# Performance work log

Measured on AMD Instinct MI355X. Metric: run time of the kernel, lower is better.

Reference implementation:

```python
import jax, jax.numpy as jnp
import numpy as np

NU = 3
NUM_MEM_TOKENS = 128
EPS = 1e-5


def dpfp(x, nu=NU):
    # x: [..., d] -> [..., 2*nu*d]; all outputs are >= 0
    x = jnp.concatenate([jax.nn.relu(x), jax.nn.relu(-x)], axis=-1)
    x_rolled = jnp.concatenate([jnp.roll(x, shift=j, axis=-1) for j in range(1, nu + 1)], axis=-1)
    x_repeat = jnp.concatenate([x] * nu, axis=-1)
    return x_repeat * x_rolled


def setup_inputs() -> dict:
    key = jax.random.key(0)
    ks = jax.random.split(key, 8)
    B, S, D, DM = 1, 16384, 2048, 64
    DK = 2 * NU * DM  # 384
    scale = 0.02
    return {
        "hidden_states": jax.random.normal(ks[0], (B, S, D), jnp.float32),
        "Wmq": jax.random.normal(ks[1], (DM, D), jnp.float32) * scale,
        "Wmk": jax.random.normal(ks[2], (DM, D), jnp.float32) * scale,
        "Wmv": jax.random.normal(ks[3], (D, D), jnp.float32) * scale,
        "Wmb_w": jax.random.normal(ks[4], (1, D), jnp.float32) * scale,
        "Wmb_b": jax.random.normal(ks[5], (1,), jnp.float32),
        "W_mem": jax.random.normal(ks[6], (B, DK, D), jnp.float32) * scale,
        "z": jax.random.uniform(ks[7], (B, DK), jnp.float32) + 0.1,
    }


def reference(hidden_states, Wmq, Wmk, Wmv, Wmb_w, Wmb_b, W_mem, z):
    # ---- associate (read from fast-weight memory) ----
    mq = dpfp(hidden_states @ Wmq.T)                       # [b,s,dk]
    num = jnp.einsum('ijk,ikt->ijt', mq, W_mem)            # [b,s,d]
    denom = jnp.einsum('ik,ijk->ij', z, mq)[..., None] + EPS
    hidden_states = num / denom + hidden_states

    # wrapped transformer layer modeled as identity
    out = hidden_states

    # ---- update_mem (write: recurrent outer-product accumulation) ----
    mem_tokens = out[:, -NUM_MEM_TOKENS:]                  # [b,m,d]
    mk = dpfp(mem_tokens @ Wmk.T)                          # [b,m,dk]
    new_mv = mem_tokens @ Wmv.T                            # [b,m,d]

    num2 = jnp.einsum('ijk,ikt->ijt', mk, W_mem)           # [b,m,d]
    denom2 = jnp.einsum('ij,ikj->ik', z, mk)[..., None] + EPS
    prev_mv = num2 / denom2

    mk_sq = jnp.sum(mk * mk, axis=-1)                      # ||mk||^2, [b,m]
    new_info_coef = 1.0 - denom2 / (mk_sq + EPS)[..., None]
    new_info_coef = jax.lax.stop_gradient(jnp.clip(new_info_coef, 0.0, 1.0))

    mv = new_mv - prev_mv
    mb = jax.nn.sigmoid(mem_tokens @ Wmb_w.T + Wmb_b)[..., 0]  # [b,m]
    associations = jnp.einsum('ijk,ijt,ij->ikt', mk, mv, mb)   # [b,dk,d]

    W_mem_new = W_mem + associations
    z_new = z + jnp.sum(new_info_coef * mk, axis=1)
    return out, W_mem_new, z_new
```

## Files before the change

kernel.cpp:

```cpp
#include <hip/hip_runtime.h>
#include <hip/hip_bf16.h>
#include <math.h>

#define S_ 16384
#define D_ 2048
#define DM_ 64
#define DK_ 384
#define NMEM_ 128
#define EPS_ 1e-5f

typedef __attribute__((ext_vector_type(8))) short bf16x8;
typedef __attribute__((ext_vector_type(8))) short s16x8;
typedef __attribute__((ext_vector_type(4))) float f32x4;
typedef unsigned short u16;

static __device__ __forceinline__ u16 f2bf(float x) {
    __hip_bfloat16 h = __float2bfloat16(x);
    return *reinterpret_cast<u16*>(&h);
}

static __device__ __forceinline__ void gload16(const void* g, void* l) {
    __builtin_amdgcn_global_load_lds(
        (const __attribute__((address_space(1))) unsigned int*)g,
        (__attribute__((address_space(3))) unsigned int*)l, 16, 0, 0);
}

__global__ __launch_bounds__(256) void k_qprep(const float* __restrict__ hs,
                                               const float* __restrict__ Wmq,
                                               const float* __restrict__ Wmv,
                                               const float* __restrict__ Wmem,
                                               const float* __restrict__ z,
                                               u16* __restrict__ Wmv_b,
                                               u16* __restrict__ WmT,
                                               u16* __restrict__ mq_b,
                                               float* __restrict__ denomv) {
    __shared__ float ts[32][33];
    __shared__ u16 As[32 * 128];
    __shared__ u16 Bs[64 * 128];
    __shared__ float xs[32][128];
    __shared__ float zs[DK_];
    const int bid = blockIdx.x;
    const int tid = threadIdx.x;
    if (bid < 4096) {
        size_t idx = ((size_t)bid * 256 + tid) * 4;
        float4 v = *reinterpret_cast<const float4*>(&Wmv[idx]);
        ushort4 p;
        p.x = f2bf(v.x); p.y = f2bf(v.y); p.z = f2bf(v.z); p.w = f2bf(v.w);
        *reinterpret_cast<ushort4*>(&Wmv_b[idx]) = p;
        return;
    }
    if (bid < 4864) {
        int t = bid - 4096;
        int c0 = (t & 63) * 32, k0 = (t >> 6) * 32;
        const int tx = tid & 31, ty = tid >> 5;
#pragma unroll
        for (int i = 0; i < 4; ++i)
            ts[ty + 8 * i][tx] = Wmem[(size_t)(k0 + ty + 8 * i) * D_ + c0 + tx];
        __syncthreads();
#pragma unroll
        for (int i = 0; i < 4; ++i)
            WmT[(size_t)(c0 + ty + 8 * i) * DK_ + k0 + tx] = f2bf(ts[tx][ty + 8 * i]);
        return;
    }
    const int r0 = (bid - 4864) * 32;
    const int lane = tid & 63, w = tid >> 6;
    const int lrow = lane & 15, lkg = lane >> 4;
    const int wr = w >> 1, wc = w & 1;
    for (int i = tid; i < DK_; i += 256) zs[i] = z[i];
    f32x4 acc[2];
    const f32x4 zero4 = {0.f, 0.f, 0.f, 0.f};
    acc[0] = zero4; acc[1] = zero4;
    for (int kc = 0; kc < D_ / 128; ++kc) {
#pragma unroll
        for (int i = 0; i < 4; ++i) {
            int flat4 = tid + 256 * i;
            int row = flat4 >> 5, c4 = flat4 & 31;
            const float4 v = *reinterpret_cast<const float4*>(
                &hs[(size_t)(r0 + row) * D_ + kc * 128 + c4 * 4]);
            int off = row * 128 + (((c4 >> 1) ^ (row & 7)) * 8) + (c4 & 1) * 4;
            ushort4 p;
            p.x = f2bf(v.x); p.y = f2bf(v.y); p.z = f2bf(v.z); p.w = f2bf(v.w);
            *reinterpret_cast<ushort4*>(&As[off]) = p;
        }
#pragma unroll
        for (int i = 0; i < 8; ++i) {
            int flat4 = tid + 256 * i;
            int row = flat4 >> 5, c4 = flat4 & 31;
            const float4 v = *reinterpret_cast<const float4*>(
                &Wmq[(size_t)row * D_ + kc * 128 + c4 * 4]);
            int off = row * 128 + (((c4 >> 1) ^ (row & 7)) * 8) + (c4 & 1) * 4;
            ushort4 p;
            p.x = f2bf(v.x); p.y = f2bf(v.y); p.z = f2bf(v.z); p.w = f2bf(v.w);
            *reinterpret_cast<ushort4*>(&Bs[off]) = p;
        }
        __syncthreads();
#pragma unroll
        for (int s = 0; s < 4; ++s) {
            int rl = wr * 16 + lrow;
            bf16x8 a_ = *reinterpret_cast<const bf16x8*>(
                &As[rl * 128 + (((s * 4 + lkg) ^ (rl & 7)) * 8)]);
#pragma unroll
            for (int n = 0; n < 2; ++n) {
                int cl = wc * 32 + n * 16 + lrow;
                bf16x8 b_ = *reinterpret_cast<const bf16x8*>(
                    &Bs[cl * 128 + (((s * 4 + lkg) ^ (cl & 7)) * 8)]);
                acc[n] = __builtin_amdgcn_mfma_f32_16x16x32_bf16(a_, b_, acc[n], 0, 0, 0);
            }
        }
        __syncthreads();
    }
#pragma unroll
    for (int n = 0; n < 2; ++n) {
        int col = wc * 32 + n * 16 + lrow;
#pragma unroll
        for (int r = 0; r < 4; ++r) {
            int row = wr * 16 + lkg * 4 + r;
            float q = acc[n][r];
            xs[row][col] = fmaxf(q, 0.f);
            xs[row][col + 64] = fmaxf(-q, 0.f);
        }
    }
    __syncthreads();
    {
        int row = tid >> 3, sub = tid & 7;
        float pd = 0.f;
#pragma unroll
        for (int c = 0; c < 6; ++c) {
            int base = sub * 48 + c * 8;
            int g = base >> 7;
            s16x8 pk;
#pragma unroll
            for (int e = 0; e < 8; ++e) {
                int m = base + e;
                int i = m & 127;
                float v = xs[row][i] * xs[row][(i - g - 1) & 127];
                pd += zs[m] * v;
                pk[e] = (short)f2bf(v);
            }
            *reinterpret_cast<s16x8*>(&mq_b[(size_t)(r0 + row) * DK_ + base]) = pk;
        }
        pd += __shfl_down(pd, 4, 8);
        pd += __shfl_down(pd, 2, 8);
        pd += __shfl_down(pd, 1, 8);
        if (sub == 0) denomv[r0 + row] = pd + EPS_;
    }
}

__global__ __launch_bounds__(256) void k_main(const float* __restrict__ hs,
                                              const u16* __restrict__ mq_b,
                                              const u16* __restrict__ WmT,
                                              const float* __restrict__ denomv,
                                              float* __restrict__ out) {
    __shared__ u16 At[128 * 64];
    __shared__ u16 Bt[128 * 64];
    __shared__ float dinv[128];
    const int bid = blockIdx.x;
    const int swz = (bid & 7) * 256 + (bid >> 3);
    const int r0 = (swz >> 4) * 128, c0 = (swz & 15) * 128;
    const int tid = threadIdx.x;
    const int lane = tid & 63, w = tid >> 6;
    const int lrow = lane & 15, lkg = lane >> 4;
    const int wr = w >> 1, wc = w & 1;
    if (tid < 128) dinv[tid] = 1.f / denomv[r0 + tid];
    f32x4 acc[4][4];
    const f32x4 zero4 = {0.f, 0.f, 0.f, 0.f};
#pragma unroll
    for (int m = 0; m < 4; ++m)
#pragma unroll
        for (int n = 0; n < 4; ++n) acc[m][n] = zero4;
    for (int kc = 0; kc < 6; ++kc) {
#pragma unroll
        for (int i = 0; i < 4; ++i) {
            int rr = w * 32 + i * 8 + (lane >> 3);
            int gg = (lane & 7) ^ (rr & 7);
            gload16(mq_b + (size_t)(r0 + rr) * DK_ + kc * 64 + gg * 8,
                    &At[(w * 32 + i * 8) * 64]);
            gload16(WmT + (size_t)(c0 + rr) * DK_ + kc * 64 + gg * 8,
                    &Bt[(w * 32 + i * 8) * 64]);
        }
        __syncthreads();
#pragma unroll
        for (int s = 0; s < 2; ++s) {
            bf16x8 af[4], bb[4];
#pragma unroll
            for (int m = 0; m < 4; ++m) {
                int rl = wr * 64 + m * 16 + lrow;
                af[m] = *reinterpret_cast<const bf16x8*>(
                    &At[rl * 64 + (((s * 4 + lkg) ^ (rl & 7)) * 8)]);
            }
#pragma unroll
            for (int n = 0; n < 4; ++n) {
                int cl = wc * 64 + n * 16 + lrow;
                bb[n] = *reinterpret_cast<const bf16x8*>(
                    &Bt[cl * 64 + (((s * 4 + lkg) ^ (cl & 7)) * 8)]);
            }
#pragma unroll
            for (int m = 0; m < 4; ++m)
#pragma unroll
                for (int n = 0; n < 4; ++n)
                    acc[m][n] = __builtin_amdgcn_mfma_f32_16x16x32_bf16(
                        af[m], bb[n], acc[m][n], 0, 0, 0);
        }
        __syncthreads();
    }
#pragma unroll
    for (int m = 0; m < 4; ++m)
#pragma unroll
        for (int n = 0; n < 4; ++n) {
            int colg = c0 + wc * 64 + n * 16 + lrow;
#pragma unroll
            for (int r = 0; r < 4; ++r) {
                int rowl = wr * 64 + m * 16 + lkg * 4 + r;
                size_t off = (size_t)(r0 + rowl) * D_ + colg;
                out[off] = acc[m][n][r] * dinv[rowl] + hs[off];
            }
        }
}

__global__ __launch_bounds__(256) void k_mk(const float* __restrict__ out,
                                            const float* __restrict__ Wmk,
                                            const float* __restrict__ Wmb_w,
                                            const float* __restrict__ Wmb_b,
                                            const float* __restrict__ z,
                                            float* __restrict__ mk_g,
                                            u16* __restrict__ mk_b,
                                            u16* __restrict__ mem_b,
                                            float* __restrict__ scal) {
    __shared__ float memRow[D_];
    __shared__ float qpart[4][64];
    __shared__ float xv[128];
    __shared__ float mks[DK_];
    __shared__ float red[256];
    const int j = blockIdx.x;
    const int tid = threadIdx.x;
    const float* mem = out + (size_t)(S_ - NMEM_ + j) * D_;
    const float4* mem4 = reinterpret_cast<const float4*>(mem);
    float4* mr4 = reinterpret_cast<float4*>(memRow);
#pragma unroll
    for (int i4 = tid; i4 < 512; i4 += 256) {
        float4 v = mem4[i4];
        mr4[i4] = v;
        ushort4 p;
        p.x = f2bf(v.x); p.y = f2bf(v.y); p.z = f2bf(v.z); p.w = f2bf(v.w);
        *reinterpret_cast<ushort4*>(&mem_b[(size_t)j * D_ + i4 * 4]) = p;
    }
    __syncthreads();
    {
        int c = tid & 63, seg = tid >> 6;
        const float4* wrow = reinterpret_cast<const float4*>(Wmk + (size_t)c * D_);
        float p = 0.f;
#pragma unroll 4
        for (int k4 = seg * 128; k4 < seg * 128 + 128; ++k4) {
            float4 a = mr4[k4], b = wrow[k4];
            p += a.x * b.x + a.y * b.y + a.z * b.z + a.w * b.w;
        }
        qpart[seg][c] = p;
    }
    __syncthreads();
    if (tid < 64) {
        float q = qpart[0][tid] + qpart[1][tid] + qpart[2][tid] + qpart[3][tid];
        xv[tid] = fmaxf(q, 0.f);
        xv[tid + 64] = fmaxf(-q, 0.f);
    }
    __syncthreads();
    for (int m = tid; m < DK_; m += 256) {
        int i = m & 127, g = m >> 7;
        float v = xv[i] * xv[(i - g - 1) & 127];
        mks[m] = v;
        mk_g[(size_t)j * DK_ + m] = v;
        mk_b[(size_t)j * DK_ + m] = f2bf(v);
    }
    __syncthreads();
    float pd = 0.f, ps = 0.f;
    for (int m = tid; m < DK_; m += 256) { float v = mks[m]; pd += v * z[m]; ps += v * v; }
    red[tid] = pd; __syncthreads();
    for (int s = 128; s > 0; s >>= 1) { if (tid < s) red[tid] += red[tid + s]; __syncthreads(); }
    float denom2 = red[0] + EPS_;
    __syncthreads();
    red[tid] = ps; __syncthreads();
    for (int s = 128; s > 0; s >>= 1) { if (tid < s) red[tid] += red[tid + s]; __syncthreads(); }
    float mksq = red[0];
    __syncthreads();
    float pb = 0.f;
    {
        const float4* wb4 = reinterpret_cast<const float4*>(Wmb_w);
#pragma unroll
        for (int k4 = tid; k4 < 512; k4 += 256) {
            float4 a = mr4[k4], b = wb4[k4];
            pb += a.x * b.x + a.y * b.y + a.z * b.z + a.w * b.w;
        }
    }
    red[tid] = pb; __syncthreads();
    for (int s = 128; s > 0; s >>= 1) { if (tid < s) red[tid] += red[tid + s]; __syncthreads(); }
    if (tid == 0) {
        float bsum = red[0] + Wmb_b[0];
        float mb = 1.f / (1.f + expf(-bsum));
        float nic = 1.f - denom2 / (mksq + EPS_);
        nic = fminf(fmaxf(nic, 0.f), 1.f);
        scal[j * 4 + 0] = denom2;
        scal[j * 4 + 1] = nic;
        scal[j * 4 + 2] = mb;
        scal[j * 4 + 3] = mksq;
    }
}

__global__ __launch_bounds__(256) void k_mv(const u16* __restrict__ mem_b,
                                            const u16* __restrict__ Wmv_b,
                                            const u16* __restrict__ mk_b,
                                            const u16* __restrict__ WmT,
                                            const float* __restrict__ scal,
                                            float* __restrict__ mvb) {
    __shared__ u16 At[128 * 64];
    __shared__ u16 Bt[64 * 64];
    __shared__ float inv2[128];
    __shared__ float mbl[128];
    const int c0 = blockIdx.x * 64;
    const int tid = threadIdx.x;
    const int lane = tid & 63, w = tid >> 6;
    const int lrow = lane & 15, lkg = lane >> 4;
    const int wr = w >> 1, wc = w & 1;
    if (tid < 128) {
        inv2[tid] = 1.f / scal[tid * 4 + 0];
        mbl[tid] = scal[tid * 4 + 2];
    }
    f32x4 acc1[4][2], acc2[4][2];
    const f32x4 zero4 = {0.f, 0.f, 0.f, 0.f};
#pragma unroll
    for (int m = 0; m < 4; ++m)
#pragma unroll
        for (int n = 0; n < 2; ++n) { acc1[m][n] = zero4; acc2[m][n] = zero4; }
    for (int kc = 0; kc < D_ / 64; ++kc) {
#pragma unroll
        for (int i = 0; i < 4; ++i) {
            int rr = w * 32 + i * 8 + (lane >> 3);
            int gg = (lane & 7) ^ (rr & 7);
            gload16(mem_b + (size_t)rr * D_ + kc * 64 + gg * 8,
                    &At[(w * 32 + i * 8) * 64]);
        }
#pragma unroll
        for (int i = 0; i < 2; ++i) {
            int cc = w * 16 + i * 8 + (lane >> 3);
            int gg = (lane & 7) ^ (cc & 7);
            gload16(Wmv_b + (size_t)(c0 + cc) * D_ + kc * 64 + gg * 8,
                    &Bt[(w * 16 + i * 8) * 64]);
        }
        __syncthreads();
#pragma unroll
        for (int s = 0; s < 2; ++s) {
            bf16x8 af[4], bb[2];
#pragma unroll
            for (int m = 0; m < 4; ++m) {
                int rl = wr * 64 + m * 16 + lrow;
                af[m] = *reinterpret_cast<const bf16x8*>(
                    &At[rl * 64 + (((s * 4 + lkg) ^ (rl & 7)) * 8)]);
            }
#pragma unroll
            for (int n = 0; n < 2; ++n) {
                int cl = wc * 32 + n * 16 + lrow;
                bb[n] = *reinterpret_cast<const bf16x8*>(
                    &Bt[cl * 64 + (((s * 4 + lkg) ^ (cl & 7)) * 8)]);
            }
#pragma unroll
            for (int m = 0; m < 4; ++m)
#pragma unroll
                for (int n = 0; n < 2; ++n)
                    acc1[m][n] = __builtin_amdgcn_mfma_f32_16x16x32_bf16(
                        af[m], bb[n], acc1[m][n], 0, 0, 0);
        }
        __syncthreads();
    }
    for (int kc = 0; kc < 6; ++kc) {
#pragma unroll
        for (int i = 0; i < 4; ++i) {
            int rr = w * 32 + i * 8 + (lane >> 3);
            int gg = (lane & 7) ^ (rr & 7);
            gload16(mk_b + (size_t)rr * DK_ + kc * 64 + gg * 8,
                    &At[(w * 32 + i * 8) * 64]);
        }
#pragma unroll
        for (int i = 0; i < 2; ++i) {
            int cc = w * 16 + i * 8 + (lane >> 3);
            int gg = (lane & 7) ^ (cc & 7);
            gload16(WmT + (size_t)(c0 + cc) * DK_ + kc * 64 + gg * 8,
                    &Bt[(w * 16 + i * 8) * 64]);
        }
        __syncthreads();
#pragma unroll
        for (int s = 0; s < 2; ++s) {
            bf16x8 af[4], bb[2];
#pragma unroll
            for (int m = 0; m < 4; ++m) {
                int rl = wr * 64 + m * 16 + lrow;
                af[m] = *reinterpret_cast<const bf16x8*>(
                    &At[rl * 64 + (((s * 4 + lkg) ^ (rl & 7)) * 8)]);
            }
#pragma unroll
            for (int n = 0; n < 2; ++n) {
                int cl = wc * 32 + n * 16 + lrow;
                bb[n] = *reinterpret_cast<const bf16x8*>(
                    &Bt[cl * 64 + (((s * 4 + lkg) ^ (cl & 7)) * 8)]);
            }
#pragma unroll
            for (int m = 0; m < 4; ++m)
#pragma unroll
                for (int n = 0; n < 2; ++n)
                    acc2[m][n] = __builtin_amdgcn_mfma_f32_16x16x32_bf16(
                        af[m], bb[n], acc2[m][n], 0, 0, 0);
        }
        __syncthreads();
    }
#pragma unroll
    for (int m = 0; m < 4; ++m)
#pragma unroll
        for (int n = 0; n < 2; ++n) {
            int colg = c0 + wc * 32 + n * 16 + lrow;
#pragma unroll
            for (int r = 0; r < 4; ++r) {
                int j = wr * 64 + m * 16 + lkg * 4 + r;
                mvb[(size_t)j * D_ + colg] =
                    (acc1[m][n][r] - acc2[m][n][r] * inv2[j]) * mbl[j];
            }
        }
}

__global__ __launch_bounds__(256) void k_wmem(const float* __restrict__ Wmem,
                                              const float* __restrict__ mk_g,
                                              const float* __restrict__ mvb,
                                              const float* __restrict__ scal,
                                              const float* __restrict__ z,
                                              float* __restrict__ wout,
                                              float* __restrict__ zout) {
    const int tid = threadIdx.x;
    if (blockIdx.y == 48) {
        if (blockIdx.x == 0) {
            for (int t = tid; t < DK_; t += 256) {
                float acc = z[t];
                for (int j = 0; j < NMEM_; ++j)
                    acc += scal[j * 4 + 1] * mk_g[(size_t)j * DK_ + t];
                zout[t] = acc;
            }
        }
        return;
    }
    const int c0 = blockIdx.x * 256;
    const int k0 = blockIdx.y * 8;
    const int tk = tid >> 5, tt = tid & 31;
    const float4* mvb4 = reinterpret_cast<const float4*>(mvb);
    f32x4 acc[2] = {{0.f, 0.f, 0.f, 0.f}, {0.f, 0.f, 0.f, 0.f}};
#pragma unroll 4
    for (int j = 0; j < NMEM_; ++j) {
        float a = mk_g[(size_t)j * DK_ + k0 + tk];
#pragma unroll
        for (int i = 0; i < 2; ++i) {
            float4 v = mvb4[((size_t)j * D_ + c0 + tt * 4 + 128 * i) >> 2];
            acc[i][0] += a * v.x; acc[i][1] += a * v.y;
            acc[i][2] += a * v.z; acc[i][3] += a * v.w;
        }
    }
#pragma unroll
    for (int i = 0; i < 2; ++i) {
        size_t off = (size_t)(k0 + tk) * D_ + c0 + tt * 4 + 128 * i;
        float4 wv = *reinterpret_cast<const float4*>(&Wmem[off]);
        float4 o;
        o.x = wv.x + acc[i][0]; o.y = wv.y + acc[i][1];
        o.z = wv.z + acc[i][2]; o.w = wv.w + acc[i][3];
        *reinterpret_cast<float4*>(&wout[off]) = o;
    }
}

extern "C" void kernel_launch(void* const* d_in, const int* in_sizes, int n_in,
                              void* d_out, int out_size, void* d_ws, size_t ws_size,
                              hipStream_t stream) {
    const float* hs   = (const float*)d_in[0];
    const float* Wmq  = (const float*)d_in[1];
    const float* Wmk  = (const float*)d_in[2];
    const float* Wmv  = (const float*)d_in[3];
    const float* Wmbw = (const float*)d_in[4];
    const float* Wmbb = (const float*)d_in[5];
    const float* Wmem = (const float*)d_in[6];
    const float* z    = (const float*)d_in[7];
    float* out  = (float*)d_out;
    float* wout = out + (size_t)S_ * D_;
    float* zout = wout + (size_t)DK_ * D_;

    float* ws = (float*)d_ws;
    float* denomv = ws;
    float* mk_g   = denomv + S_;
    float* scal   = mk_g + (size_t)NMEM_ * DK_;
    float* mvb    = scal + NMEM_ * 4;
    u16* mq_b  = (u16*)(mvb + (size_t)NMEM_ * D_);
    u16* WmT   = mq_b + (size_t)S_ * DK_;
    u16* Wmv_b = WmT + (size_t)D_ * DK_;
    u16* mem_b = Wmv_b + (size_t)D_ * D_;
    u16* mk_b  = mem_b + (size_t)NMEM_ * D_;

    k_qprep<<<dim3(4864 + S_ / 32), 256, 0, stream>>>(hs, Wmq, Wmv, Wmem, z,
                                                      Wmv_b, WmT, mq_b, denomv);
    k_main<<<dim3((S_ / 128) * (D_ / 128)), 256, 0, stream>>>(hs, mq_b, WmT, denomv, out);
    k_mk<<<dim3(NMEM_), 256, 0, stream>>>(out, Wmk, Wmbw, Wmbb, z, mk_g, mk_b, mem_b, scal);
    k_mv<<<dim3(D_ / 64), 256, 0, stream>>>(mem_b, Wmv_b, mk_b, WmT, scal, mvb);
    k_wmem<<<dim3(D_ / 256, DK_ / 8 + 1), 256, 0, stream>>>(Wmem, mk_g, mvb, scal, z, wout, zout);
}
```

Before: 209.0 us.

## Load q-projection operands straight from global into registers, drop LDS staging

The q-projection part of k_qprep no longer stages hs and Wmq tiles through shared memory with two barriers per K step. Each wave now owns 16 rows and reads its MFMA fragments straight from global memory into registers, converting to bf16 on the fly. Each block covers 64 rows instead of 32. The ReLU scratch is now stored as bf16 per wave, which cuts LDS use and may raise occupancy. In exchange, the global loads are strided per lane with no cross-wave sharing of the Wmq reads, and the extra bf16 rounding of the intermediate adds a little precision loss.

```diff
diff --git a/kernel.cpp b/kernel.cpp
--- a/kernel.cpp
+++ b/kernel.cpp
@@ -17,6 +17,21 @@
 static __device__ __forceinline__ u16 f2bf(float x) {
     __hip_bfloat16 h = __float2bfloat16(x);
     return *reinterpret_cast<u16*>(&h);
+}
+
+static __device__ __forceinline__ float bf2f(u16 u) {
+    unsigned int x = ((unsigned int)u) << 16;
+    union { unsigned int i; float f; } c; c.i = x;
+    return c.f;
+}
+
+static __device__ __forceinline__ bf16x8 cvt8(float4 a0, float4 a1) {
+    bf16x8 r;
+    r[0] = (short)f2bf(a0.x); r[1] = (short)f2bf(a0.y);
+    r[2] = (short)f2bf(a0.z); r[3] = (short)f2bf(a0.w);
+    r[4] = (short)f2bf(a1.x); r[5] = (short)f2bf(a1.y);
+    r[6] = (short)f2bf(a1.z); r[7] = (short)f2bf(a1.w);
+    return r;
 }
 
 static __device__ __forceinline__ void gload16(const void* g, void* l) {
@@ -35,9 +50,7 @@
                                                u16* __restrict__ mq_b,
                                                float* __restrict__ denomv) {
     __shared__ float ts[32][33];
-    __shared__ u16 As[32 * 128];
-    __shared__ u16 Bs[64 * 128];
-    __shared__ float xs[32][128];
+    __shared__ u16 xs[4][16][136];
     __shared__ float zs[DK_];
     const int bid = blockIdx.x;
     const int tid = threadIdx.x;
@@ -62,87 +75,75 @@
             WmT[(size_t)(c0 + ty + 8 * i) * DK_ + k0 + tx] = f2bf(ts[tx][ty + 8 * i]);
         return;
     }
-    const int r0 = (bid - 4864) * 32;
+    const int qb = bid - 4864;
     const int lane = tid & 63, w = tid >> 6;
     const int lrow = lane & 15, lkg = lane >> 4;
-    const int wr = w >> 1, wc = w & 1;
+    const int r0w = qb * 64 + w * 16;
     for (int i = tid; i < DK_; i += 256) zs[i] = z[i];
-    f32x4 acc[2];
+    const float* __restrict__ ap  = hs + (size_t)(r0w + lrow) * D_ + lkg * 8;
+    const float* __restrict__ bp0 = Wmq + (size_t)lrow * D_ + lkg * 8;
+    const float* __restrict__ bp1 = bp0 + (size_t)16 * D_;
+    const float* __restrict__ bp2 = bp0 + (size_t)32 * D_;
+    const float* __restrict__ bp3 = bp0 + (size_t)48 * D_;
+    f32x4 acc[4];
     const f32x4 zero4 = {0.f, 0.f, 0.f, 0.f};
-    acc[0] = zero4; acc[1] = zero4;
-    for (int kc = 0; kc < D_ / 128; ++kc) {
-#pragma unroll
-        for (int i = 0; i < 4; ++i) {
-            int flat4 = tid + 256 * i;
-            int row = flat4 >> 5, c4 = flat4 & 31;
-            const float4 v = *reinterpret_cast<const float4*>(
-                &hs[(size_t)(r0 + row) * D_ + kc * 128 + c4 * 4]);
-            int off = row * 128 + (((c4 >> 1) ^ (row & 7)) * 8) + (c4 & 1) * 4;
-            ushort4 p;
-            p.x = f2bf(v.x); p.y = f2bf(v.y); p.z = f2bf(v.z); p.w = f2bf(v.w);
-            *reinterpret_cast<ushort4*>(&As[off]) = p;
-        }
-#pragma unroll
-        for (int i = 0; i < 8; ++i) {
-            int flat4 = tid + 256 * i;
-            int row = flat4 >> 5, c4 = flat4 & 31;
-            const float4 v = *reinterpret_cast<const float4*>(
-                &Wmq[(size_t)row * D_ + kc * 128 + c4 * 4]);
-            int off = row * 128 + (((c4 >> 1) ^ (row & 7)) * 8) + (c4 & 1) * 4;
-            ushort4 p;
-            p.x = f2bf(v.x); p.y = f2bf(v.y); p.z = f2bf(v.z); p.w = f2bf(v.w);
-            *reinterpret_cast<ushort4*>(&Bs[off]) = p;
-        }
-        __syncthreads();
-#pragma unroll
-        for (int s = 0; s < 4; ++s) {
-            int rl = wr * 16 + lrow;
-            bf16x8 a_ = *reinterpret_cast<const bf16x8*>(
-                &As[rl * 128 + (((s * 4 + lkg) ^ (rl & 7)) * 8)]);
-#pragma unroll
-            for (int n = 0; n < 2; ++n) {
-                int cl = wc * 32 + n * 16 + lrow;
-                bf16x8 b_ = *reinterpret_cast<const bf16x8*>(
-                    &Bs[cl * 128 + (((s * 4 + lkg) ^ (cl & 7)) * 8)]);
-                acc[n] = __builtin_amdgcn_mfma_f32_16x16x32_bf16(a_, b_, acc[n], 0, 0, 0);
-            }
-        }
-        __syncthreads();
-    }
-#pragma unroll
-    for (int n = 0; n < 2; ++n) {
-        int col = wc * 32 + n * 16 + lrow;
+#pragma unroll
+    for (int n = 0; n < 4; ++n) acc[n] = zero4;
+#pragma unroll 4
+    for (int kk = 0; kk < 64; ++kk) {
+        const int k0 = kk * 32;
+        float4 a0 = *reinterpret_cast<const float4*>(ap + k0);
+        float4 a1 = *reinterpret_cast<const float4*>(ap + k0 + 4);
+        float4 b00 = *reinterpret_cast<const float4*>(bp0 + k0);
+        float4 b01 = *reinterpret_cast<const float4*>(bp0 + k0 + 4);
+        float4 b10 = *reinterpret_cast<const float4*>(bp1 + k0);
+        float4 b11 = *reinterpret_cast<const float4*>(bp1 + k0 + 4);
+        float4 b20 = *reinterpret_cast<const float4*>(bp2 + k0);
+        float4 b21 = *reinterpret_cast<const float4*>(bp2 + k0 + 4);
+        float4 b30 = *reinterpret_cast<const float4*>(bp3 + k0);
+        float4 b31 = *reinterpret_cast<const float4*>(bp3 + k0 + 4);
+        bf16x8 af = cvt8(a0, a1);
+        acc[0] = __builtin_amdgcn_mfma_f32_16x16x32_bf16(af, cvt8(b00, b01), acc[0], 0, 0, 0);
+        acc[1] = __builtin_amdgcn_mfma_f32_16x16x32_bf16(af, cvt8(b10, b11), acc[1], 0, 0, 0);
+        acc[2] = __builtin_amdgcn_mfma_f32_16x16x32_bf16(af, cvt8(b20, b21), acc[2], 0, 0, 0);
+        acc[3] = __builtin_amdgcn_mfma_f32_16x16x32_bf16(af, cvt8(b30, b31), acc[3], 0, 0, 0);
+    }
+#pragma unroll
+    for (int n = 0; n < 4; ++n) {
+        int col = n * 16 + lrow;
 #pragma unroll
         for (int r = 0; r < 4; ++r) {
-            int row = wr * 16 + lkg * 4 + r;
+            int row = lkg * 4 + r;
             float q = acc[n][r];
-            xs[row][col] = fmaxf(q, 0.f);
-            xs[row][col + 64] = fmaxf(-q, 0.f);
+            xs[w][row][col] = f2bf(fmaxf(q, 0.f));
+            xs[w][row][col + 64] = f2bf(fmaxf(-q, 0.f));
         }
     }
     __syncthreads();
     {
-        int row = tid >> 3, sub = tid & 7;
+        int row = tid >> 2, sub = tid & 3;
+        int wv = row >> 4, rr = row & 15;
         float pd = 0.f;
 #pragma unroll
-        for (int c = 0; c < 6; ++c) {
-            int base = sub * 48 + c * 8;
+        for (int c = 0; c < 12; ++c) {
+            int base = sub * 96 + c * 8;
             int g = base >> 7;
             s16x8 pk;
 #pragma unroll
             for (int e = 0; e < 8; ++e) {
                 int m = base + e;
                 int i = m & 127;
-                float v = xs[row][i] * xs[row][(i - g - 1) & 127];
+                float xi = bf2f(xs[wv][rr][i]);
+                float xj = bf2f(xs[wv][rr][(i - g - 1) & 127]);
+                float v = xi * xj;
                 pd += zs[m] * v;
                 pk[e] = (short)f2bf(v);
             }
-            *reinterpret_cast<s16x8*>(&mq_b[(size_t)(r0 + row) * DK_ + base]) = pk;
-        }
-        pd += __shfl_down(pd, 4, 8);
-        pd += __shfl_down(pd, 2, 8);
-        pd += __shfl_down(pd, 1, 8);
-        if (sub == 0) denomv[r0 + row] = pd + EPS_;
+            *reinterpret_cast<s16x8*>(&mq_b[(size_t)(qb * 64 + row) * DK_ + base]) = pk;
+        }
+        pd += __shfl_down(pd, 2, 4);
+        pd += __shfl_down(pd, 1, 4);
+        if (sub == 0) denomv[qb * 64 + row] = pd + EPS_;
     }
 }
 
@@ -494,7 +495,7 @@
     u16* mem_b = Wmv_b + (size_t)D_ * D_;
     u16* mk_b  = mem_b + (size_t)NMEM_ * D_;
 
-    k_qprep<<<dim3(4864 + S_ / 32), 256, 0, stream>>>(hs, Wmq, Wmv, Wmem, z,
+    k_qprep<<<dim3(4864 + S_ / 64), 256, 0, stream>>>(hs, Wmq, Wmv, Wmem, z,
                                                       Wmv_b, WmT, mq_b, denomv);
     k_main<<<dim3((S_ / 128) * (D_ / 128)), 256, 0, stream>>>(hs, mq_b, WmT, denomv, out);
     k_mk<<<dim3(NMEM_), 256, 0, stream>>>(out, Wmk, Wmbw, Wmbb, z, mk_g, mk_b, mem_b, scal);
```

After: 363.9 us. 74.1% more time.

## Pre-convert Wmq to bf16 and load it via direct global-to-LDS copies

Applied to the files above, without the earlier changes.

Splits the fused prep kernel into a weight-conversion kernel (now also converting Wmq to bf16) and a separate mq/DPFP kernel. Each block of the mq kernel previously re-read and converted the fp32 Wmq slice on every K step. Now it loads pre-converted bf16 Wmq with global_load_lds, and the K chunk is halved to 64, which shrinks LDS use. This saves redundant conversion and bandwidth across 512 blocks. In exchange it adds one more kernel launch and serialises the weight conversion before the mq computation.

```diff
diff --git a/kernel.cpp b/kernel.cpp
--- a/kernel.cpp
+++ b/kernel.cpp
@@ -25,20 +25,13 @@
         (__attribute__((address_space(3))) unsigned int*)l, 16, 0, 0);
 }
 
-__global__ __launch_bounds__(256) void k_qprep(const float* __restrict__ hs,
-                                               const float* __restrict__ Wmq,
-                                               const float* __restrict__ Wmv,
-                                               const float* __restrict__ Wmem,
-                                               const float* __restrict__ z,
-                                               u16* __restrict__ Wmv_b,
-                                               u16* __restrict__ WmT,
-                                               u16* __restrict__ mq_b,
-                                               float* __restrict__ denomv) {
+__global__ __launch_bounds__(256) void k_prep(const float* __restrict__ Wmq,
+                                              const float* __restrict__ Wmv,
+                                              const float* __restrict__ Wmem,
+                                              u16* __restrict__ Wmq_b,
+                                              u16* __restrict__ Wmv_b,
+                                              u16* __restrict__ WmT) {
     __shared__ float ts[32][33];
-    __shared__ u16 As[32 * 128];
-    __shared__ u16 Bs[64 * 128];
-    __shared__ float xs[32][128];
-    __shared__ float zs[DK_];
     const int bid = blockIdx.x;
     const int tid = threadIdx.x;
     if (bid < 4096) {
@@ -47,10 +40,14 @@
         ushort4 p;
         p.x = f2bf(v.x); p.y = f2bf(v.y); p.z = f2bf(v.z); p.w = f2bf(v.w);
         *reinterpret_cast<ushort4*>(&Wmv_b[idx]) = p;
-        return;
-    }
-    if (bid < 4864) {
-        int t = bid - 4096;
+    } else if (bid < 4224) {
+        int idx = ((bid - 4096) * 256 + tid) * 4;
+        float4 v = *reinterpret_cast<const float4*>(&Wmq[idx]);
+        ushort4 p;
+        p.x = f2bf(v.x); p.y = f2bf(v.y); p.z = f2bf(v.z); p.w = f2bf(v.w);
+        *reinterpret_cast<ushort4*>(&Wmq_b[idx]) = p;
+    } else {
+        int t = bid - 4224;
         int c0 = (t & 63) * 32, k0 = (t >> 6) * 32;
         const int tx = tid & 31, ty = tid >> 5;
 #pragma unroll
@@ -60,9 +57,20 @@
 #pragma unroll
         for (int i = 0; i < 4; ++i)
             WmT[(size_t)(c0 + ty + 8 * i) * DK_ + k0 + tx] = f2bf(ts[tx][ty + 8 * i]);
-        return;
-    }
-    const int r0 = (bid - 4864) * 32;
+    }
+}
+
+__global__ __launch_bounds__(256) void k_qdp(const float* __restrict__ hs,
+                                             const u16* __restrict__ Wmq_b,
+                                             const float* __restrict__ z,
+                                             u16* __restrict__ mq_b,
+                                             float* __restrict__ denomv) {
+    __shared__ u16 As[32 * 64];
+    __shared__ u16 Bs[64 * 64];
+    __shared__ float xs[32][128];
+    __shared__ float zs[DK_];
+    const int r0 = blockIdx.x * 32;
+    const int tid = threadIdx.x;
     const int lane = tid & 63, w = tid >> 6;
     const int lrow = lane & 15, lkg = lane >> 4;
     const int wr = w >> 1, wc = w & 1;
@@ -70,40 +78,36 @@
     f32x4 acc[2];
     const f32x4 zero4 = {0.f, 0.f, 0.f, 0.f};
     acc[0] = zero4; acc[1] = zero4;
-    for (int kc = 0; kc < D_ / 128; ++kc) {
-#pragma unroll
-        for (int i = 0; i < 4; ++i) {
+    for (int kc = 0; kc < D_ / 64; ++kc) {
+#pragma unroll
+        for (int i = 0; i < 2; ++i) {
             int flat4 = tid + 256 * i;
-            int row = flat4 >> 5, c4 = flat4 & 31;
+            int row = flat4 >> 4, c4 = flat4 & 15;
             const float4 v = *reinterpret_cast<const float4*>(
-                &hs[(size_t)(r0 + row) * D_ + kc * 128 + c4 * 4]);
-            int off = row * 128 + (((c4 >> 1) ^ (row & 7)) * 8) + (c4 & 1) * 4;
+                &hs[(size_t)(r0 + row) * D_ + kc * 64 + c4 * 4]);
+            int off = row * 64 + (((c4 >> 1) ^ (row & 7)) * 8) + (c4 & 1) * 4;
             ushort4 p;
             p.x = f2bf(v.x); p.y = f2bf(v.y); p.z = f2bf(v.z); p.w = f2bf(v.w);
             *reinterpret_cast<ushort4*>(&As[off]) = p;
         }
 #pragma unroll
-        for (int i = 0; i < 8; ++i) {
-            int flat4 = tid + 256 * i;
-            int row = flat4 >> 5, c4 = flat4 & 31;
-            const float4 v = *reinterpret_cast<const float4*>(
-                &Wmq[(size_t)row * D_ + kc * 128 + c4 * 4]);
-            int off = row * 128 + (((c4 >> 1) ^ (row & 7)) * 8) + (c4 & 1) * 4;
-            ushort4 p;
-            p.x = f2bf(v.x); p.y = f2bf(v.y); p.z = f2bf(v.z); p.w = f2bf(v.w);
-            *reinterpret_cast<ushort4*>(&Bs[off]) = p;
-        }
-        __syncthreads();
-#pragma unroll
-        for (int s = 0; s < 4; ++s) {
+        for (int i = 0; i < 2; ++i) {
+            int col = w * 16 + i * 8 + (lane >> 3);
+            int gg = (lane & 7) ^ (col & 7);
+            gload16(Wmq_b + (size_t)col * D_ + kc * 64 + gg * 8,
+                    &Bs[(w * 16 + i * 8) * 64]);
+        }
+        __syncthreads();
+#pragma unroll
+        for (int s = 0; s < 2; ++s) {
             int rl = wr * 16 + lrow;
             bf16x8 a_ = *reinterpret_cast<const bf16x8*>(
-                &As[rl * 128 + (((s * 4 + lkg) ^ (rl & 7)) * 8)]);
+                &As[rl * 64 + (((s * 4 + lkg) ^ (rl & 7)) * 8)]);
 #pragma unroll
             for (int n = 0; n < 2; ++n) {
                 int cl = wc * 32 + n * 16 + lrow;
                 bf16x8 b_ = *reinterpret_cast<const bf16x8*>(
-                    &Bs[cl * 128 + (((s * 4 + lkg) ^ (cl & 7)) * 8)]);
+                    &Bs[cl * 64 + (((s * 4 + lkg) ^ (cl & 7)) * 8)]);
                 acc[n] = __builtin_amdgcn_mfma_f32_16x16x32_bf16(a_, b_, acc[n], 0, 0, 0);
             }
         }
@@ -490,12 +494,13 @@
     float* mvb    = scal + NMEM_ * 4;
     u16* mq_b  = (u16*)(mvb + (size_t)NMEM_ * D_);
     u16* WmT   = mq_b + (size_t)S_ * DK_;
-    u16* Wmv_b = WmT + (size_t)D_ * DK_;
+    u16* Wmq_b = WmT + (size_t)D_ * DK_;
+    u16* Wmv_b = Wmq_b + (size_t)DM_ * D_;
     u16* mem_b = Wmv_b + (size_t)D_ * D_;
     u16* mk_b  = mem_b + (size_t)NMEM_ * D_;
 
-    k_qprep<<<dim3(4864 + S_ / 32), 256, 0, stream>>>(hs, Wmq, Wmv, Wmem, z,
-                                                      Wmv_b, WmT, mq_b, denomv);
+    k_prep<<<dim3(4992), 256, 0, stream>>>(Wmq, Wmv, Wmem, Wmq_b, Wmv_b, WmT);
+    k_qdp<<<dim3(S_ / 32), 256, 0, stream>>>(hs, Wmq_b, z, mq_b, denomv);
     k_main<<<dim3((S_ / 128) * (D_ / 128)), 256, 0, stream>>>(hs, mq_b, WmT, denomv, out);
     k_mk<<<dim3(NMEM_), 256, 0, stream>>>(out, Wmk, Wmbw, Wmbb, z, mk_g, mk_b, mem_b, scal);
     k_mv<<<dim3(D_ / 64), 256, 0, stream>>>(mem_b, Wmv_b, mk_b, WmT, scal, mvb);
```

New measurement: 198.2 us (median of 2 runs). 5.2% less time.
